# Performance work log

Hardware: AMD Instinct MI355X
Metric: run time of the kernel (lower is better)

## Reference

```python
import jax, jax.numpy as jnp
import numpy as np
from jax import lax

T, R, W, F_CWT, E, H, HG, NC, K = 16, 200, 50, 32, 128, 256, 256, 2, 20


def _make_wavelets():
    t = np.linspace(-1.0, 1.0, W)
    w0 = 6.0
    freqs = np.linspace(1.0, W / 2.0, F_CWT)
    wr = np.zeros((F_CWT, 1, W), np.float32)
    wi = np.zeros((F_CWT, 1, W), np.float32)
    for i, s in enumerate(freqs):
        norm = s ** (-0.5) * np.pi ** (-0.25)
        ts = t / s
        psi = norm * np.exp(1j * w0 * ts) * np.exp(-0.5 * ts ** 2)
        wr[i, 0] = psi.real.astype(np.float32)
        wi[i, 0] = psi.imag.astype(np.float32)
    return jnp.asarray(wr), jnp.asarray(wi)


def setup_inputs() -> dict:
    key = jax.random.key(0)
    ks = jax.random.split(key, 20)
    wr, wi = _make_wavelets()
    s = 0.05
    inp = {
        "time_windows": jax.random.normal(ks[0], (T, R, W), jnp.float32),
        "wav_real": wr, "wav_imag": wi,
        "conv1_w": jax.random.normal(ks[1], (16, 1, 3, 3), jnp.float32) * s,
        "conv1_b": jnp.zeros((16,), jnp.float32),
        "bn1_g": jnp.ones((16,), jnp.float32), "bn1_b": jnp.zeros((16,), jnp.float32),
        "conv2_w": jax.random.normal(ks[2], (32, 16, 3, 3), jnp.float32) * s,
        "conv2_b": jnp.zeros((32,), jnp.float32),
        "bn2_g": jnp.ones((32,), jnp.float32), "bn2_b": jnp.zeros((32,), jnp.float32),
        "fc_w": jax.random.normal(ks[3], (E, 32), jnp.float32) * s,
        "fc_b": jnp.zeros((E,), jnp.float32),
        "q_w": jax.random.normal(ks[4], (E, E), jnp.float32) * s,
        "q_b": jnp.zeros((E,), jnp.float32),
        "k_w": jax.random.normal(ks[5], (E, E), jnp.float32) * s,
        "k_b": jnp.zeros((E,), jnp.float32),
        "gcn1_w": jax.random.normal(ks[6], (E, H), jnp.float32) * s,
        "gcn1_b": jnp.zeros((H,), jnp.float32),
        "gcn2_w": jax.random.normal(ks[7], (H, H), jnp.float32) * s,
        "gcn2_b": jnp.zeros((H,), jnp.float32),
        "gru_wih": jax.random.normal(ks[8], (3 * HG, H), jnp.float32) * s,
        "gru_whh": jax.random.normal(ks[9], (3 * HG, HG), jnp.float32) * s,
        "gru_bih": jnp.zeros((3 * HG,), jnp.float32),
        "gru_bhh": jnp.zeros((3 * HG,), jnp.float32),
        "cls_w": jax.random.normal(ks[10], (NC, HG), jnp.float32) * s,
        "cls_b": jnp.zeros((NC,), jnp.float32),
    }
    return inp


def _conv_bn_relu_pool(x, w, b, g, beta):
    # conv2d k3 pad1, training-mode BN, relu, maxpool2 (floor)
    x = lax.conv_general_dilated(x, w, (1, 1), ((1, 1), (1, 1)),
                                 dimension_numbers=("NCHW", "OIHW", "NCHW"))
    x = x + b[None, :, None, None]
    mu = x.mean((0, 2, 3), keepdims=True)
    var = x.var((0, 2, 3), keepdims=True)
    x = (x - mu) * lax.rsqrt(var + 1e-5) * g[None, :, None, None] + beta[None, :, None, None]
    x = jax.nn.relu(x)
    return lax.reduce_window(x, -jnp.inf, lax.max, (1, 1, 2, 2), (1, 1, 2, 2), "VALID")


def _forward(time_windows, wav_real, wav_imag, conv1_w, conv1_b, bn1_g, bn1_b,
             conv2_w, conv2_b, bn2_g, bn2_b, fc_w, fc_b, q_w, q_b, k_w, k_b,
             gcn1_w, gcn1_b, gcn2_w, gcn2_b, gru_wih, gru_whh, gru_bih, gru_bhh,
             cls_w, cls_b):
    N = T * R
    x = time_windows.reshape(N, 1, W)
    pl = (W - 1) // 2
    pr = (W - 1) - pl  # torch padding='same' (extra on right)
    re = lax.conv_general_dilated(x, wav_real, (1,), [(pl, pr)],
                                  dimension_numbers=("NCH", "OIH", "NCH"))
    im = lax.conv_general_dilated(x, wav_imag, (1,), [(pl, pr)],
                                  dimension_numbers=("NCH", "OIH", "NCH"))
    scal = jnp.sqrt(re * re + im * im)              # [N, F_CWT, W]

    h = scal[:, None]                               # [N,1,F,W]
    h = _conv_bn_relu_pool(h, conv1_w, conv1_b, bn1_g, bn1_b)
    h = _conv_bn_relu_pool(h, conv2_w, conv2_b, bn2_g, bn2_b)
    pooled = h.mean((2, 3))                         # adaptive avg pool -> [N,32]
    emb = pooled @ fc_w.T + fc_b                    # [N,E]
    emb = emb.reshape(T, R, E)

    # sparse-attention graph generation (per window, vectorized over T)
    Q = emb @ q_w.T + q_b
    Kp = emb @ k_w.T + k_b
    attn = jnp.einsum("tre,tse->trs", Q, Kp) / (E ** 0.5)
    attn = jax.nn.leaky_relu(attn, 0.2)
    _, idx = lax.top_k(attn, K)                     # [T,R,K]
    mask = jnp.zeros_like(attn).at[
        jnp.arange(T)[:, None, None], jnp.arange(R)[None, :, None], idx].set(1.0)
    masked = attn * mask
    masked = jnp.where(masked == 0.0, -1e9, masked)
    adj = jax.nn.softmax(masked, axis=-1)           # [T,R,R] row-stochastic, topk-sparse

    # GCNConv x2 with edge weights (PyG gcn_norm: remaining self-loops weight 1,
    ii = jnp.arange(R)
    diag = adj[:, ii, ii]
    adj_sl = adj.at[:, ii, ii].set(jnp.where(diag == 0.0, 1.0, diag))
    Bm = jnp.swapaxes(adj_sl, 1, 2)
    deg = Bm.sum(-1)
    dinv = jnp.where(deg > 0, deg, 1.0) ** -0.5
    An = dinv[:, :, None] * Bm * dinv[:, None, :]   # [T,R,R]
    g = jax.nn.relu(jnp.einsum("trs,tsh->trh", An, emb @ gcn1_w) + gcn1_b)
    g = jax.nn.relu(jnp.einsum("trs,tsh->trh", An, g @ gcn2_w) + gcn2_b)
    g_emb = g.mean(1)                               # [T,H]

    # GRU over the T graph embeddings (batch 1, gate order r,z,n)
    def step(hprev, xt):
        gi = xt @ gru_wih.T + gru_bih
        gh = hprev @ gru_whh.T + gru_bhh
        ir, iz, inn = jnp.split(gi, 3)
        hr, hz, hn = jnp.split(gh, 3)
        r = jax.nn.sigmoid(ir + hr)
        z = jax.nn.sigmoid(iz + hz)
        n = jnp.tanh(inn + r * hn)
        return (1.0 - z) * n + z * hprev, None

    hT, _ = lax.scan(step, jnp.zeros((HG,), emb.dtype), g_emb)
    pred = (hT @ cls_w.T + cls_b)[None]             # [1,NC]

    edge_var = jnp.mean(jnp.var(adj, axis=0, ddof=1))
    avg_adj = adj.mean(0)[None]                     # [1,R,R]
    return pred, avg_adj, edge_var


def reference(time_windows, wav_real, wav_imag, conv1_w, conv1_b, bn1_g, bn1_b,
              conv2_w, conv2_b, bn2_g, bn2_b, fc_w, fc_b, q_w, q_b, k_w, k_b,
              gcn1_w, gcn1_b, gcn2_w, gcn2_b, gru_wih, gru_whh, gru_bih, gru_bhh,
              cls_w, cls_b):
    return _forward(time_windows, wav_real, wav_imag, conv1_w, conv1_b, bn1_g, bn1_b,
                    conv2_w, conv2_b, bn2_g, bn2_b, fc_w, fc_b, q_w, q_b, k_w, k_b,
                    gcn1_w, gcn1_b, gcn2_w, gcn2_b, gru_wih, gru_whh, gru_bih, gru_bhh,
                    cls_w, cls_b)
```

## Files before the change

kernel.cpp:

```cpp
#include <hip/hip_runtime.h>
#include <cfloat>
#include <cmath>

#define T_ 16
#define R_ 200
#define W_ 50
#define FCWT 32
#define E_ 128
#define K_ 20
#define N_ 3200

__device__ __forceinline__ void waveReduce2(float& a, float& b) {
#pragma unroll
    for (int o = 32; o > 0; o >>= 1) {
        a += __shfl_down(a, o, 64);
        b += __shfl_down(b, o, 64);
    }
}

__global__ __launch_bounds__(256) void cwt_conv1_stats_kernel(const float* __restrict__ x,
                                                              const float* __restrict__ wr,
                                                              const float* __restrict__ wi,
                                                              const float* __restrict__ w1,
                                                              const float* __restrict__ b1,
                                                              float* __restrict__ scal,
                                                              double* __restrict__ psum,
                                                              double* __restrict__ psq) {
    int n = blockIdx.x, tid = threadIdx.x;
    __shared__ float sx[W_];
    __shared__ float swr[FCWT * W_];
    __shared__ float swi[FCWT * W_];
    __shared__ float P1[34 * 52];
    __shared__ float ls[256], lq[256];
    if (tid < W_) sx[tid] = x[n * W_ + tid];
    for (int idx = tid; idx < FCWT * W_; idx += 256) { swr[idx] = wr[idx]; swi[idx] = wi[idx]; }
    for (int idx = tid; idx < 34 * 52; idx += 256) P1[idx] = 0.f;
    __syncthreads();
    for (int idx = tid; idx < 1600; idx += 256) {
        int f = idx / 50, i = idx % 50;
        int jlo = (24 - i) > 0 ? (24 - i) : 0;
        int jhi = (73 - i) < 49 ? (73 - i) : 49;
        float re = 0.f, im = 0.f;
        for (int j = jlo; j <= jhi; ++j) {
            float xv = sx[i + j - 24];
            re += xv * swr[f * 50 + j];
            im += xv * swi[f * 50 + j];
        }
        float v = sqrtf(re * re + im * im);
        scal[n * 1600 + idx] = v;
        P1[(f + 1) * 52 + (i + 1)] = v;
    }
    __syncthreads();
    int c = tid & 15, pgq = tid >> 4;
    float wv[9];
#pragma unroll
    for (int j = 0; j < 9; ++j) wv[j] = w1[c * 9 + j];
    float bias = b1[c];
    float s = 0.f, q = 0.f;
    for (int k = 0; k < 100; ++k) {
        int pos = pgq + 16 * k;
        int y = pos / 50, xx = pos % 50;
        const float* p = &P1[y * 52 + xx];
        float v = bias + p[0] * wv[0] + p[1] * wv[1] + p[2] * wv[2]
                       + p[52] * wv[3] + p[53] * wv[4] + p[54] * wv[5]
                       + p[104] * wv[6] + p[105] * wv[7] + p[106] * wv[8];
        s += v; q += v * v;
    }
    ls[tid] = s; lq[tid] = q;
    __syncthreads();
    if (tid < 16) {
        float ss = 0.f, qq = 0.f;
        for (int g = 0; g < 16; ++g) { ss += ls[tid + 16 * g]; qq += lq[tid + 16 * g]; }
        psum[n * 16 + tid] = (double)ss;
        psq[n * 16 + tid] = (double)qq;
    }
}

__global__ __launch_bounds__(256) void bn_finalize_kernel(const double* __restrict__ psum,
                                                          const double* __restrict__ psq,
                                                          const float* __restrict__ g,
                                                          const float* __restrict__ beta,
                                                          float* __restrict__ scale,
                                                          float* __restrict__ shift,
                                                          int C, double inv_count) {
    int c = blockIdx.x, tid = threadIdx.x;
    double s = 0.0, q = 0.0;
    for (int n = tid; n < N_; n += 256) { s += psum[n * C + c]; q += psq[n * C + c]; }
#pragma unroll
    for (int o = 32; o > 0; o >>= 1) { s += __shfl_down(s, o, 64); q += __shfl_down(q, o, 64); }
    __shared__ double sa[4], sb[4];
    int lane = tid & 63, wid = tid >> 6;
    if (lane == 0) { sa[wid] = s; sb[wid] = q; }
    __syncthreads();
    if (tid == 0) {
        s = sa[0] + sa[1] + sa[2] + sa[3];
        q = sb[0] + sb[1] + sb[2] + sb[3];
        double mu = s * inv_count;
        double var = q * inv_count - mu * mu;
        double rstd = 1.0 / sqrt(var + 1e-5);
        double gg = (double)g[c];
        scale[c] = (float)(gg * rstd);
        shift[c] = (float)((double)beta[c] - mu * rstd * gg);
    }
}

__global__ __launch_bounds__(256) void conv1_norm_pool_kernel(const float* __restrict__ scal,
                                                              const float* __restrict__ w1,
                                                              const float* __restrict__ b1,
                                                              const float* __restrict__ scale,
                                                              const float* __restrict__ shift,
                                                              float* __restrict__ pooled1) {
    int n = blockIdx.x, tid = threadIdx.x;
    __shared__ float P1[34 * 52];
    for (int idx = tid; idx < 34 * 52; idx += 256) {
        int yy = idx / 52, xx = idx % 52;
        float v = 0.f;
        if (yy >= 1 && yy <= 32 && xx >= 1 && xx <= 50)
            v = scal[n * 1600 + (yy - 1) * 50 + (xx - 1)];
        P1[idx] = v;
    }
    __syncthreads();
    int c = tid >> 4, sub = tid & 15;
    float wv[9];
#pragma unroll
    for (int j = 0; j < 9; ++j) wv[j] = w1[c * 9 + j];
    float bias = b1[c], sc = scale[c], sh = shift[c];
    for (int k = 0; k < 25; ++k) {
        int cell = sub + 16 * k;
        int py = cell / 25, px = cell % 25;
        int y0 = 2 * py, x0 = 2 * px;
        float p[4][4];
#pragma unroll
        for (int iy = 0; iy < 4; ++iy)
#pragma unroll
            for (int ix = 0; ix < 4; ++ix)
                p[iy][ix] = P1[(y0 + iy) * 52 + x0 + ix];
        float m = -FLT_MAX;
#pragma unroll
        for (int dy = 0; dy < 2; ++dy)
#pragma unroll
            for (int dx = 0; dx < 2; ++dx) {
                float acc = bias;
#pragma unroll
                for (int ky = 0; ky < 3; ++ky)
#pragma unroll
                    for (int kx = 0; kx < 3; ++kx)
                        acc += p[dy + ky][dx + kx] * wv[ky * 3 + kx];
                m = fmaxf(m, acc * sc + sh);
            }
        pooled1[((n * 16 + c) * 16 + py) * 25 + px] = fmaxf(m, 0.f);
    }
}

__global__ __launch_bounds__(256) void conv2_compute_kernel(const float* __restrict__ pooled1,
                                                            const float* __restrict__ w2,
                                                            const float* __restrict__ b2,
                                                            float* __restrict__ mm,
                                                            double* __restrict__ psum,
                                                            double* __restrict__ psq,
                                                            int store_min) {
    int n = blockIdx.x, tid = threadIdx.x;
    __shared__ float P2[16 * 18 * 27];
    __shared__ float swT[144 * 32];
    __shared__ float ls[256], lq[256];
    for (int idx = tid; idx < 16 * 18 * 27; idx += 256) {
        int ci = idx / 486, rem = idx % 486, yy = rem / 27, xx = rem % 27;
        float v = 0.f;
        if (yy >= 1 && yy <= 16 && xx >= 1 && xx <= 25)
            v = pooled1[((n * 16 + ci) * 16 + (yy - 1)) * 25 + (xx - 1)];
        P2[idx] = v;
    }
    for (int idx = tid; idx < 4608; idx += 256) {
        int co = idx / 144, r = idx % 144;
        swT[r * 32 + co] = w2[idx];
    }
    __syncthreads();
    int co = tid & 31, pg = tid >> 5;
    float bias = b2[co];
    float s = 0.f, q = 0.f;
    int stride = store_min ? 64 : 32;
    for (int kk = 0; kk < 4; ++kk) {
        int task = pg + 8 * kk;
        int pr = task >> 2, cb = task & 3;
        int y0 = 2 * pr, x0 = 6 * cb;
        float a[2][6];
#pragma unroll
        for (int r2 = 0; r2 < 2; ++r2)
#pragma unroll
            for (int xi = 0; xi < 6; ++xi) a[r2][xi] = bias;
        for (int ci = 0; ci < 16; ++ci) {
            const float* base = &P2[ci * 486];
            const float* wb = &swT[(ci * 9) * 32 + co];
#pragma unroll
            for (int iy = 0; iy < 4; ++iy) {
                const float* row = &base[(y0 + iy) * 27 + x0];
                float r0 = row[0], r1 = row[1], r2v = row[2], r3 = row[3];
                float r4 = row[4], r5 = row[5], r6 = row[6], r7 = row[7];
                if (iy < 3) {
                    float w0 = wb[(iy * 3 + 0) * 32], w1 = wb[(iy * 3 + 1) * 32], w2v = wb[(iy * 3 + 2) * 32];
                    a[0][0] += r0 * w0 + r1 * w1 + r2v * w2v;
                    a[0][1] += r1 * w0 + r2v * w1 + r3 * w2v;
                    a[0][2] += r2v * w0 + r3 * w1 + r4 * w2v;
                    a[0][3] += r3 * w0 + r4 * w1 + r5 * w2v;
                    a[0][4] += r4 * w0 + r5 * w1 + r6 * w2v;
                    a[0][5] += r5 * w0 + r6 * w1 + r7 * w2v;
                }
                if (iy >= 1) {
                    int ky = iy - 1;
                    float w0 = wb[(ky * 3 + 0) * 32], w1 = wb[(ky * 3 + 1) * 32], w2v = wb[(ky * 3 + 2) * 32];
                    a[1][0] += r0 * w0 + r1 * w1 + r2v * w2v;
                    a[1][1] += r1 * w0 + r2v * w1 + r3 * w2v;
                    a[1][2] += r2v * w0 + r3 * w1 + r4 * w2v;
                    a[1][3] += r3 * w0 + r4 * w1 + r5 * w2v;
                    a[1][4] += r4 * w0 + r5 * w1 + r6 * w2v;
                    a[1][5] += r5 * w0 + r6 * w1 + r7 * w2v;
                }
            }
        }
#pragma unroll
        for (int r2 = 0; r2 < 2; ++r2)
#pragma unroll
            for (int xi = 0; xi < 6; ++xi) { float v = a[r2][xi]; s += v; q += v * v; }
#pragma unroll
        for (int pc = 0; pc < 3; ++pc) {
            float v00 = a[0][2 * pc], v01 = a[0][2 * pc + 1];
            float v10 = a[1][2 * pc], v11 = a[1][2 * pc + 1];
            float mx = fmaxf(fmaxf(v00, v01), fmaxf(v10, v11));
            int cellIdx = pr * 12 + 3 * cb + pc;
            mm[((size_t)n * 96 + cellIdx) * stride + co] = mx;
            if (store_min) {
                float mn = fminf(fminf(v00, v01), fminf(v10, v11));
                mm[((size_t)n * 96 + cellIdx) * 64 + 32 + co] = mn;
            }
        }
    }
    {
        int y0 = 2 * pg;
        float a0 = bias, a1 = bias;
        for (int ci = 0; ci < 16; ++ci) {
            const float* base = &P2[ci * 486];
            const float* wb = &swT[(ci * 9) * 32 + co];
#pragma unroll
            for (int iy = 0; iy < 4; ++iy) {
                const float* row = &base[(y0 + iy) * 27 + 24];
                float r0 = row[0], r1 = row[1], r2v = row[2];
                if (iy < 3) {
                    float w0 = wb[(iy * 3 + 0) * 32], w1 = wb[(iy * 3 + 1) * 32], w2v = wb[(iy * 3 + 2) * 32];
                    a0 += r0 * w0 + r1 * w1 + r2v * w2v;
                }
                if (iy >= 1) {
                    int ky = iy - 1;
                    float w0 = wb[(ky * 3 + 0) * 32], w1 = wb[(ky * 3 + 1) * 32], w2v = wb[(ky * 3 + 2) * 32];
                    a1 += r0 * w0 + r1 * w1 + r2v * w2v;
                }
            }
        }
        s += a0 + a1; q += a0 * a0 + a1 * a1;
    }
    ls[tid] = s; lq[tid] = q;
    __syncthreads();
    if (tid < 32) {
        float ss = 0.f, qq = 0.f;
        for (int g2 = 0; g2 < 8; ++g2) { ss += ls[tid + 32 * g2]; qq += lq[tid + 32 * g2]; }
        psum[n * 32 + tid] = (double)ss;
        psq[n * 32 + tid] = (double)qq;
    }
}

__global__ __launch_bounds__(256) void pool_mean_kernel(const float* __restrict__ mm,
                                                        const float* __restrict__ scale,
                                                        const float* __restrict__ shift,
                                                        float* __restrict__ pm,
                                                        int store_min) {
    int n = blockIdx.x, tid = threadIdx.x;
    int co = tid & 31, grp = tid >> 5;
    float sc = scale[co], sh = shift[co];
    int stride = store_min ? 64 : 32;
    float acc = 0.f;
    for (int j = 0; j < 12; ++j) {
        int cell = grp * 12 + j;
        float v;
        if (store_min && sc < 0.f) {
            float mn = mm[((size_t)n * 96 + cell) * 64 + 32 + co];
            v = mn * sc + sh;
        } else {
            float mx = mm[((size_t)n * 96 + cell) * stride + co];
            v = mx * sc + sh;
        }
        acc += fmaxf(v, 0.f);
    }
    __shared__ float red[256];
    red[tid] = acc;
    __syncthreads();
    if (tid < 32) {
        float t = 0.f;
        for (int g = 0; g < 8; ++g) t += red[co + 32 * g];
        pm[n * 32 + co] = t * (1.f / 96.f);
    }
}

__global__ __launch_bounds__(128) void fc_kernel(const float* __restrict__ pm,
                                                 const float* __restrict__ fc_w,
                                                 const float* __restrict__ fc_b,
                                                 float* __restrict__ emb) {
    int n = blockIdx.x, e = threadIdx.x;
    __shared__ float sp[32];
    if (e < 32) sp[e] = pm[n * 32 + e];
    __syncthreads();
    const float* w = fc_w + e * 32;
    float acc = fc_b[e];
    for (int c = 0; c < 32; ++c) acc += sp[c] * w[c];
    emb[n * 128 + e] = acc;
}

__global__ __launch_bounds__(128) void qk_kernel(const float* __restrict__ emb,
                                                 const float* __restrict__ q_w,
                                                 const float* __restrict__ q_b,
                                                 const float* __restrict__ k_w,
                                                 const float* __restrict__ k_b,
                                                 float* __restrict__ Q,
                                                 float* __restrict__ Kp) {
    int n = blockIdx.x, e = threadIdx.x;
    const float* w = (blockIdx.y == 0) ? q_w : k_w;
    const float* b = (blockIdx.y == 0) ? q_b : k_b;
    float* out = (blockIdx.y == 0) ? Q : Kp;
    __shared__ float se[128];
    se[e] = emb[n * 128 + e];
    __syncthreads();
    const float* wr = w + e * 128;
    float acc = b[e];
    for (int k = 0; k < 128; ++k) acc += se[k] * wr[k];
    out[n * 128 + e] = acc;
}

__global__ __launch_bounds__(256) void attn_kernel(const float* __restrict__ Q,
                                                   const float* __restrict__ Kp,
                                                   float* __restrict__ attn) {
    int r = blockIdx.x, t = blockIdx.y, tid = threadIdx.x;
    __shared__ float sq[128];
    if (tid < 128) sq[tid] = Q[(t * 200 + r) * 128 + tid];
    __syncthreads();
    if (tid < 200) {
        const float4* kp4 = (const float4*)(Kp + (size_t)(t * 200 + tid) * 128);
        float acc = 0.f;
#pragma unroll 8
        for (int e4 = 0; e4 < 32; ++e4) {
            float4 k4 = kp4[e4];
            acc += sq[e4 * 4 + 0] * k4.x + sq[e4 * 4 + 1] * k4.y +
                   sq[e4 * 4 + 2] * k4.z + sq[e4 * 4 + 3] * k4.w;
        }
        acc = acc / 11.313708498984761f;
        acc = (acc >= 0.f) ? acc : 0.2f * acc;
        attn[(size_t)(t * 200 + r) * 200 + tid] = acc;
    }
}

__global__ __launch_bounds__(64) void topk_softmax_kernel(const float* __restrict__ attn,
                                                          float* __restrict__ adj) {
    int row = blockIdx.x;
    int lane = threadIdx.x;
    const float* a = attn + (size_t)row * 200;
    float v[4], w[4];
#pragma unroll
    for (int j = 0; j < 4; ++j) {
        int i = lane + 64 * j;
        float x = (i < 200) ? a[i] : -FLT_MAX;
        v[j] = x; w[j] = x;
    }
    unsigned sel = 0;
    for (int it = 0; it < K_; ++it) {
        float best = -FLT_MAX; int bidx = 0x7fffffff;
#pragma unroll
        for (int j = 0; j < 4; ++j) {
            int i = lane + 64 * j;
            if (w[j] > best || (w[j] == best && i < bidx)) { best = w[j]; bidx = i; }
        }
#pragma unroll
        for (int off = 32; off > 0; off >>= 1) {
            float ob = __shfl_down(best, off, 64);
            int oi = __shfl_down(bidx, off, 64);
            if (ob > best || (ob == best && oi < bidx)) { best = ob; bidx = oi; }
        }
        bidx = __shfl(bidx, 0, 64);
        if ((bidx & 63) == lane) { int j = bidx >> 6; w[j] = -FLT_MAX; sel |= (1u << j); }
    }
    float mv[4]; float m = -FLT_MAX;
#pragma unroll
    for (int j = 0; j < 4; ++j) {
        int i = lane + 64 * j;
        float x = -1e9f;
        if (i < 200 && ((sel >> j) & 1u)) x = (v[j] == 0.f) ? -1e9f : v[j];
        mv[j] = x; m = fmaxf(m, x);
    }
#pragma unroll
    for (int off = 32; off > 0; off >>= 1) m = fmaxf(m, __shfl_xor(m, off, 64));
    float s = 0.f; float e[4];
#pragma unroll
    for (int j = 0; j < 4; ++j) {
        int i = lane + 64 * j;
        e[j] = (i < 200) ? expf(mv[j] - m) : 0.f;
        s += e[j];
    }
#pragma unroll
    for (int off = 32; off > 0; off >>= 1) s += __shfl_xor(s, off, 64);
    float inv = 1.f / s;
#pragma unroll
    for (int j = 0; j < 4; ++j) {
        int i = lane + 64 * j;
        if (i < 200) adj[(size_t)row * 200 + i] = e[j] * inv;
    }
}

__global__ __launch_bounds__(256) void build_An_kernel(const float* __restrict__ adj,
                                                       float* __restrict__ An) {
    int t = blockIdx.x, tid = threadIdx.x;
    __shared__ float dinv[200];
    if (tid < 200) {
        float acc = 0.f;
        for (int s = 0; s < 200; ++s) {
            float v = adj[(size_t)(t * 200 + s) * 200 + tid];
            if (s == tid) v = (v == 0.f) ? 1.f : v;
            acc += v;
        }
        float d = (acc > 0.f) ? acc : 1.f;
        dinv[tid] = 1.f / sqrtf(d);
    }
    __syncthreads();
    for (int idx = tid; idx < 200 * 200; idx += 256) {
        int r = idx / 200, s = idx % 200;
        float v = adj[(size_t)(t * 200 + s) * 200 + r];
        if (s == r) v = (v == 0.f) ? 1.f : v;
        An[(size_t)(t * 200 + r) * 200 + s] = dinv[r] * v * dinv[s];
    }
}

__global__ __launch_bounds__(256) void linear_kernel(const float* __restrict__ in,
                                                     const float* __restrict__ w,
                                                     float* __restrict__ out, int IN) {
    int n = blockIdx.x, h = threadIdx.x;
    __shared__ float s[256];
    for (int i = h; i < IN; i += 256) s[i] = in[n * IN + i];
    __syncthreads();
    float acc = 0.f;
    for (int k = 0; k < IN; ++k) acc += s[k] * w[k * 256 + h];
    out[(size_t)n * 256 + h] = acc;
}

__global__ __launch_bounds__(256) void gcn_agg_kernel(const float* __restrict__ An,
                                                      const float* __restrict__ X,
                                                      const float* __restrict__ b,
                                                      float* __restrict__ out) {
    int r = blockIdx.x, t = blockIdx.y, h = threadIdx.x;
    __shared__ float sa[200];
    for (int i = h; i < 200; i += 256) sa[i] = An[(size_t)(t * 200 + r) * 200 + i];
    __syncthreads();
    const float* Xt = X + (size_t)t * 200 * 256;
    float acc = 0.f;
    for (int s = 0; s < 200; ++s) acc += sa[s] * Xt[s * 256 + h];
    out[(size_t)(t * 200 + r) * 256 + h] = fmaxf(acc + b[h], 0.f);
}

__global__ __launch_bounds__(256) void gemb_kernel(const float* __restrict__ g2,
                                                   float* __restrict__ g_emb) {
    int t = blockIdx.x, h = threadIdx.x;
    float acc = 0.f;
    for (int r = 0; r < 200; ++r) acc += g2[(size_t)(t * 200 + r) * 256 + h];
    g_emb[t * 256 + h] = acc * (1.f / 200.f);
}

__global__ __launch_bounds__(256) void transpose_768x256_kernel(const float* __restrict__ in,
                                                                float* __restrict__ outT) {
    int gid = blockIdx.x * 256 + threadIdx.x;
    int k = gid / 768, j = gid % 768;
    outT[gid] = in[j * 256 + k];
}

__global__ __launch_bounds__(768) void gi_kernel(const float* __restrict__ g_emb,
                                                 const float* __restrict__ wihT,
                                                 const float* __restrict__ bih,
                                                 float* __restrict__ GI) {
    int t = blockIdx.x, j = threadIdx.x;
    __shared__ float sg[256];
    if (j < 256) sg[j] = g_emb[t * 256 + j];
    __syncthreads();
    float acc = bih[j];
    for (int k = 0; k < 256; ++k) acc += sg[k] * wihT[k * 768 + j];
    GI[t * 768 + j] = acc;
}

__global__ __launch_bounds__(768) void gru_cls_kernel(const float* __restrict__ GI,
                                                      const float* __restrict__ whhT,
                                                      const float* __restrict__ bhh,
                                                      const float* __restrict__ cls_w,
                                                      const float* __restrict__ cls_b,
                                                      float* __restrict__ out) {
    int j = threadIdx.x;
    __shared__ float h[256];
    __shared__ float gh[768];
    __shared__ float s0[4], s1[4];
    if (j < 256) h[j] = 0.f;
    float bh = bhh[j];
    __syncthreads();
    for (int t = 0; t < 16; ++t) {
        float acc = bh;
        for (int k = 0; k < 256; ++k) acc += h[k] * whhT[k * 768 + j];
        gh[j] = acc;
        __syncthreads();
        if (j < 256) {
            float r = 1.f / (1.f + expf(-(GI[t * 768 + j] + gh[j])));
            float z = 1.f / (1.f + expf(-(GI[t * 768 + 256 + j] + gh[256 + j])));
            float nn = tanhf(GI[t * 768 + 512 + j] + r * gh[512 + j]);
            h[j] = (1.f - z) * nn + z * h[j];
        }
        __syncthreads();
    }
    float v0 = 0.f, v1 = 0.f;
    if (j < 256) { v0 = h[j] * cls_w[j]; v1 = h[j] * cls_w[256 + j]; }
    waveReduce2(v0, v1);
    int lane = j & 63, wid = j >> 6;
    if (lane == 0 && wid < 4) { s0[wid] = v0; s1[wid] = v1; }
    __syncthreads();
    if (j == 0) {
        out[0] = s0[0] + s0[1] + s0[2] + s0[3] + cls_b[0];
        out[1] = s1[0] + s1[1] + s1[2] + s1[3] + cls_b[1];
    }
}

__global__ __launch_bounds__(256) void edge_kernel(const float* __restrict__ adj,
                                                   float* __restrict__ out) {
    int gid = blockIdx.x * 256 + threadIdx.x;
    float var = 0.f;
    if (gid < 40000) {
        float v[16]; float s = 0.f;
#pragma unroll
        for (int t = 0; t < 16; ++t) { v[t] = adj[t * 40000 + gid]; s += v[t]; }
        float mean = s * (1.f / 16.f);
        float q = 0.f;
#pragma unroll
        for (int t = 0; t < 16; ++t) { float d = v[t] - mean; q += d * d; }
        var = q * (1.f / 15.f);
        out[2 + gid] = mean;
    }
    float dummy = 0.f;
    waveReduce2(var, dummy);
    __shared__ float sa[4];
    int lane = threadIdx.x & 63, wid = threadIdx.x >> 6;
    if (lane == 0) sa[wid] = var;
    __syncthreads();
    if (threadIdx.x == 0) {
        float bs = sa[0] + sa[1] + sa[2] + sa[3];
        atomicAdd(&out[40002], bs * (1.f / 40000.f));
    }
}

extern "C" void kernel_launch(void* const* d_in, const int* in_sizes, int n_in,
                              void* d_out, int out_size, void* d_ws, size_t ws_size,
                              hipStream_t stream) {
    const float* tw      = (const float*)d_in[0];
    const float* wav_r   = (const float*)d_in[1];
    const float* wav_i   = (const float*)d_in[2];
    const float* conv1_w = (const float*)d_in[3];
    const float* conv1_b = (const float*)d_in[4];
    const float* bn1_g   = (const float*)d_in[5];
    const float* bn1_b   = (const float*)d_in[6];
    const float* conv2_w = (const float*)d_in[7];
    const float* conv2_b = (const float*)d_in[8];
    const float* bn2_g   = (const float*)d_in[9];
    const float* bn2_b   = (const float*)d_in[10];
    const float* fc_w    = (const float*)d_in[11];
    const float* fc_b    = (const float*)d_in[12];
    const float* q_w     = (const float*)d_in[13];
    const float* q_b     = (const float*)d_in[14];
    const float* k_w     = (const float*)d_in[15];
    const float* k_b     = (const float*)d_in[16];
    const float* gcn1_w  = (const float*)d_in[17];
    const float* gcn1_b  = (const float*)d_in[18];
    const float* gcn2_w  = (const float*)d_in[19];
    const float* gcn2_b  = (const float*)d_in[20];
    const float* gru_wih = (const float*)d_in[21];
    const float* gru_whh = (const float*)d_in[22];
    const float* gru_bih = (const float*)d_in[23];
    const float* gru_bhh = (const float*)d_in[24];
    const float* cls_w   = (const float*)d_in[25];
    const float* cls_b   = (const float*)d_in[26];
    float* out = (float*)d_out;
    (void)in_sizes; (void)n_in; (void)out_size;

    const size_t POOLED1_B = (size_t)N_ * 16 * 16 * 25 * 4;
    const size_t SCALU_B   = (size_t)N_ * 1600 * 4;
    const size_t MM_FULL_B = (size_t)N_ * 96 * 64 * 4;
    const size_t MM_MAX_B  = (size_t)N_ * 96 * 32 * 4;
    const size_t P1S_B     = (size_t)N_ * 16 * 8;
    const size_t P2S_B     = (size_t)N_ * 32 * 8;
    const size_t WT_B      = (size_t)768 * 256 * 4;
    size_t fixed = POOLED1_B + SCALU_B + 2 * P1S_B + 2 * P2S_B + 2 * WT_B + 8 * 256 + 4096;
    int store_min = (ws_size >= fixed + MM_FULL_B) ? 1 : 0;
    const size_t MM_B = store_min ? MM_FULL_B : MM_MAX_B;

    size_t off = 0;
    char* Wb = (char*)d_ws;
    auto take = [&](size_t bytes) -> char* {
        char* p = Wb + off;
        off += (bytes + 255) & ~(size_t)255;
        return p;
    };
    float* pooled1 = (float*)take(POOLED1_B);
    char*  scalU   = take(SCALU_B);
    char*  mmU     = take(MM_B);
    double* p1sum = (double*)take(P1S_B);
    double* p1sq  = (double*)take(P1S_B);
    double* p2sum = (double*)take(P2S_B);
    double* p2sq  = (double*)take(P2S_B);
    float* scale1 = (float*)take(64 * 4);
    float* shift1 = (float*)take(64 * 4);
    float* scale2 = (float*)take(64 * 4);
    float* shift2 = (float*)take(64 * 4);
    float* wihT   = (float*)take(WT_B);
    float* whhT   = (float*)take(WT_B);

    float* scal = (float*)scalU;
    float* pm   = (float*)(scalU + 0);
    float* emb  = (float*)(scalU + 409600);
    float* Q    = (float*)(scalU + 409600 + 1638400);
    float* Kp   = (float*)(scalU + 409600 + 2 * 1638400);

    float* mm   = (float*)mmU;
    size_t moff = 0;
    auto mtake = [&](size_t bytes) -> float* {
        float* p = (float*)(mmU + moff);
        moff += (bytes + 255) & ~(size_t)255;
        return p;
    };
    float* attn  = mtake((size_t)T_ * 200 * 200 * 4);
    float* adj   = mtake((size_t)T_ * 200 * 200 * 4);
    float* An    = mtake((size_t)T_ * 200 * 200 * 4);
    float* X1    = mtake((size_t)N_ * 256 * 4);
    float* g1    = mtake((size_t)N_ * 256 * 4);
    float* X2    = mtake((size_t)N_ * 256 * 4);
    float* g2    = mtake((size_t)N_ * 256 * 4);
    float* g_emb = mtake((size_t)T_ * 256 * 4);
    float* GI    = mtake((size_t)T_ * 768 * 4);

    transpose_768x256_kernel<<<768, 256, 0, stream>>>(gru_wih, wihT);
    transpose_768x256_kernel<<<768, 256, 0, stream>>>(gru_whh, whhT);
    cwt_conv1_stats_kernel<<<N_, 256, 0, stream>>>(tw, wav_r, wav_i, conv1_w, conv1_b,
                                                   scal, p1sum, p1sq);
    bn_finalize_kernel<<<16, 256, 0, stream>>>(p1sum, p1sq, bn1_g, bn1_b, scale1, shift1,
                                               16, 1.0 / 5120000.0);
    conv1_norm_pool_kernel<<<N_, 256, 0, stream>>>(scal, conv1_w, conv1_b, scale1, shift1,
                                                   pooled1);
    conv2_compute_kernel<<<N_, 256, 0, stream>>>(pooled1, conv2_w, conv2_b, mm,
                                                 p2sum, p2sq, store_min);
    bn_finalize_kernel<<<32, 256, 0, stream>>>(p2sum, p2sq, bn2_g, bn2_b, scale2, shift2,
                                               32, 1.0 / 1280000.0);
    pool_mean_kernel<<<N_, 256, 0, stream>>>(mm, scale2, shift2, pm, store_min);
    fc_kernel<<<N_, 128, 0, stream>>>(pm, fc_w, fc_b, emb);
    qk_kernel<<<dim3(N_, 2), 128, 0, stream>>>(emb, q_w, q_b, k_w, k_b, Q, Kp);
    attn_kernel<<<dim3(200, 16), 256, 0, stream>>>(Q, Kp, attn);
    topk_softmax_kernel<<<N_, 64, 0, stream>>>(attn, adj);
    build_An_kernel<<<16, 256, 0, stream>>>(adj, An);
    linear_kernel<<<N_, 256, 0, stream>>>(emb, gcn1_w, X1, 128);
    gcn_agg_kernel<<<dim3(200, 16), 256, 0, stream>>>(An, X1, gcn1_b, g1);
    linear_kernel<<<N_, 256, 0, stream>>>(g1, gcn2_w, X2, 256);
    gcn_agg_kernel<<<dim3(200, 16), 256, 0, stream>>>(An, X2, gcn2_b, g2);
    gemb_kernel<<<16, 256, 0, stream>>>(g2, g_emb);
    gi_kernel<<<16, 768, 0, stream>>>(g_emb, wihT, gru_bih, GI);
    gru_cls_kernel<<<1, 768, 0, stream>>>(GI, whhT, gru_bhh, cls_w, cls_b, out);
    hipMemsetAsync(out + 40002, 0, sizeof(float), stream);
    edge_kernel<<<(40000 + 255) / 256, 256, 0, stream>>>(adj, out);
}
```

Before: 903.0 us.

## Restructure conv, GCN and GRU kernels for register reuse and multi-block recurrence

Rewrites the CWT as a sliding-window register computation and changes conv1 stats and conv1-pool to row-streaming sliding windows with pooled output staged in shared memory. conv2 now computes whole output rows per thread with float4 loads. Building the normalized adjacency is split into a degree kernel and a tiled transpose kernel. The linear and GCN aggregation kernels process 8 rows per block so each loaded weight or feature is reused. The GRU recurrence is spread over 6 blocks with register-resident weights and a flag-based inter-block barrier, which adds spin-wait synchronisation risk and extra register pressure.

```diff
diff --git a/kernel.cpp b/kernel.cpp
--- a/kernel.cpp
+++ b/kernel.cpp
@@ -9,6 +9,7 @@
 #define E_ 128
 #define K_ 20
 #define N_ 3200
+#define GRU_BLOCKS 6
 
 __device__ __forceinline__ void waveReduce2(float& a, float& b) {
 #pragma unroll
@@ -27,44 +28,67 @@
                                                               double* __restrict__ psum,
                                                               double* __restrict__ psq) {
     int n = blockIdx.x, tid = threadIdx.x;
-    __shared__ float sx[W_];
+    __shared__ float sxp[112];
     __shared__ float swr[FCWT * W_];
     __shared__ float swi[FCWT * W_];
     __shared__ float P1[34 * 52];
     __shared__ float ls[256], lq[256];
-    if (tid < W_) sx[tid] = x[n * W_ + tid];
+    if (tid < 112) sxp[tid] = (tid >= 24 && tid < 74) ? x[n * 50 + (tid - 24)] : 0.f;
     for (int idx = tid; idx < FCWT * W_; idx += 256) { swr[idx] = wr[idx]; swi[idx] = wi[idx]; }
     for (int idx = tid; idx < 34 * 52; idx += 256) P1[idx] = 0.f;
     __syncthreads();
+    if (tid < 64) {
+        int f = tid >> 1, i0 = (tid & 1) * 25;
+        float xw[25], ar[25], ai[25];
+#pragma unroll
+        for (int d = 0; d < 25; ++d) { xw[d] = sxp[i0 + d]; ar[d] = 0.f; ai[d] = 0.f; }
+        const float* wrf = &swr[f * 50];
+        const float* wif = &swi[f * 50];
+        for (int j = 0; j < 50; ++j) {
+            float wrv = wrf[j], wiv = wif[j];
+#pragma unroll
+            for (int d = 0; d < 25; ++d) { ar[d] += xw[d] * wrv; ai[d] += xw[d] * wiv; }
+            float xnew = sxp[i0 + j + 25];
+#pragma unroll
+            for (int d = 0; d < 24; ++d) xw[d] = xw[d + 1];
+            xw[24] = xnew;
+        }
+#pragma unroll
+        for (int d = 0; d < 25; ++d) {
+            float v = sqrtf(ar[d] * ar[d] + ai[d] * ai[d]);
+            P1[(f + 1) * 52 + (i0 + d + 1)] = v;
+        }
+    }
+    __syncthreads();
     for (int idx = tid; idx < 1600; idx += 256) {
-        int f = idx / 50, i = idx % 50;
-        int jlo = (24 - i) > 0 ? (24 - i) : 0;
-        int jhi = (73 - i) < 49 ? (73 - i) : 49;
-        float re = 0.f, im = 0.f;
-        for (int j = jlo; j <= jhi; ++j) {
-            float xv = sx[i + j - 24];
-            re += xv * swr[f * 50 + j];
-            im += xv * swi[f * 50 + j];
-        }
-        float v = sqrtf(re * re + im * im);
-        scal[n * 1600 + idx] = v;
-        P1[(f + 1) * 52 + (i + 1)] = v;
-    }
-    __syncthreads();
-    int c = tid & 15, pgq = tid >> 4;
+        int ff = idx / 50, ii = idx % 50;
+        scal[n * 1600 + idx] = P1[(ff + 1) * 52 + ii + 1];
+    }
+    int c = tid & 15, pg = tid >> 4;
     float wv[9];
 #pragma unroll
-    for (int j = 0; j < 9; ++j) wv[j] = w1[c * 9 + j];
+    for (int k = 0; k < 9; ++k) wv[k] = w1[c * 9 + k];
     float bias = b1[c];
+    const float* r0p = &P1[(2 * pg + 0) * 52];
+    const float* r1p = &P1[(2 * pg + 1) * 52];
+    const float* r2p = &P1[(2 * pg + 2) * 52];
+    const float* r3p = &P1[(2 * pg + 3) * 52];
+    float c0[4], c1[4];
+    c0[0] = r0p[0]; c0[1] = r1p[0]; c0[2] = r2p[0]; c0[3] = r3p[0];
+    c1[0] = r0p[1]; c1[1] = r1p[1]; c1[2] = r2p[1]; c1[3] = r3p[1];
     float s = 0.f, q = 0.f;
-    for (int k = 0; k < 100; ++k) {
-        int pos = pgq + 16 * k;
-        int y = pos / 50, xx = pos % 50;
-        const float* p = &P1[y * 52 + xx];
-        float v = bias + p[0] * wv[0] + p[1] * wv[1] + p[2] * wv[2]
-                       + p[52] * wv[3] + p[53] * wv[4] + p[54] * wv[5]
-                       + p[104] * wv[6] + p[105] * wv[7] + p[106] * wv[8];
-        s += v; q += v * v;
+    for (int xx = 0; xx < 50; ++xx) {
+        float c2[4];
+        c2[0] = r0p[xx + 2]; c2[1] = r1p[xx + 2]; c2[2] = r2p[xx + 2]; c2[3] = r3p[xx + 2];
+        float v0 = bias + c0[0] * wv[0] + c1[0] * wv[1] + c2[0] * wv[2]
+                        + c0[1] * wv[3] + c1[1] * wv[4] + c2[1] * wv[5]
+                        + c0[2] * wv[6] + c1[2] * wv[7] + c2[2] * wv[8];
+        float v1 = bias + c0[1] * wv[0] + c1[1] * wv[1] + c2[1] * wv[2]
+                        + c0[2] * wv[3] + c1[2] * wv[4] + c2[2] * wv[5]
+                        + c0[3] * wv[6] + c1[3] * wv[7] + c2[3] * wv[8];
+        s += v0 + v1; q += v0 * v0 + v1 * v1;
+#pragma unroll
+        for (int rr = 0; rr < 4; ++rr) { c0[rr] = c1[rr]; c1[rr] = c2[rr]; }
     }
     ls[tid] = s; lq[tid] = q;
     __syncthreads();
@@ -112,6 +136,7 @@
                                                               float* __restrict__ pooled1) {
     int n = blockIdx.x, tid = threadIdx.x;
     __shared__ float P1[34 * 52];
+    __shared__ float outb[6400];
     for (int idx = tid; idx < 34 * 52; idx += 256) {
         int yy = idx / 52, xx = idx % 52;
         float v = 0.f;
@@ -120,36 +145,37 @@
         P1[idx] = v;
     }
     __syncthreads();
-    int c = tid >> 4, sub = tid & 15;
+    int c = tid & 15, py = tid >> 4;
     float wv[9];
 #pragma unroll
-    for (int j = 0; j < 9; ++j) wv[j] = w1[c * 9 + j];
+    for (int k = 0; k < 9; ++k) wv[k] = w1[c * 9 + k];
     float bias = b1[c], sc = scale[c], sh = shift[c];
-    for (int k = 0; k < 25; ++k) {
-        int cell = sub + 16 * k;
-        int py = cell / 25, px = cell % 25;
-        int y0 = 2 * py, x0 = 2 * px;
-        float p[4][4];
-#pragma unroll
-        for (int iy = 0; iy < 4; ++iy)
-#pragma unroll
-            for (int ix = 0; ix < 4; ++ix)
-                p[iy][ix] = P1[(y0 + iy) * 52 + x0 + ix];
-        float m = -FLT_MAX;
-#pragma unroll
-        for (int dy = 0; dy < 2; ++dy)
-#pragma unroll
-            for (int dx = 0; dx < 2; ++dx) {
-                float acc = bias;
-#pragma unroll
-                for (int ky = 0; ky < 3; ++ky)
-#pragma unroll
-                    for (int kx = 0; kx < 3; ++kx)
-                        acc += p[dy + ky][dx + kx] * wv[ky * 3 + kx];
-                m = fmaxf(m, acc * sc + sh);
-            }
-        pooled1[((n * 16 + c) * 16 + py) * 25 + px] = fmaxf(m, 0.f);
-    }
+    const float* r0p = &P1[(2 * py + 0) * 52];
+    const float* r1p = &P1[(2 * py + 1) * 52];
+    const float* r2p = &P1[(2 * py + 2) * 52];
+    const float* r3p = &P1[(2 * py + 3) * 52];
+    float c0[4], c1[4];
+    c0[0] = r0p[0]; c0[1] = r1p[0]; c0[2] = r2p[0]; c0[3] = r3p[0];
+    c1[0] = r0p[1]; c1[1] = r1p[1]; c1[2] = r2p[1]; c1[3] = r3p[1];
+    float pmax = -FLT_MAX;
+    for (int xx = 0; xx < 50; ++xx) {
+        float c2[4];
+        c2[0] = r0p[xx + 2]; c2[1] = r1p[xx + 2]; c2[2] = r2p[xx + 2]; c2[3] = r3p[xx + 2];
+        float v0 = bias + c0[0] * wv[0] + c1[0] * wv[1] + c2[0] * wv[2]
+                        + c0[1] * wv[3] + c1[1] * wv[4] + c2[1] * wv[5]
+                        + c0[2] * wv[6] + c1[2] * wv[7] + c2[2] * wv[8];
+        float v1 = bias + c0[1] * wv[0] + c1[1] * wv[1] + c2[1] * wv[2]
+                        + c0[2] * wv[3] + c1[2] * wv[4] + c2[2] * wv[5]
+                        + c0[3] * wv[6] + c1[3] * wv[7] + c2[3] * wv[8];
+        float m2 = fmaxf(v0 * sc + sh, v1 * sc + sh);
+        if ((xx & 1) == 0) pmax = m2;
+        else outb[(c * 16 + py) * 25 + (xx >> 1)] = fmaxf(fmaxf(pmax, m2), 0.f);
+#pragma unroll
+        for (int rr = 0; rr < 4; ++rr) { c0[rr] = c1[rr]; c1[rr] = c2[rr]; }
+    }
+    __syncthreads();
+    for (int idx = tid; idx < 6400; idx += 256)
+        pooled1[(size_t)n * 6400 + idx] = outb[idx];
 }
 
 __global__ __launch_bounds__(256) void conv2_compute_kernel(const float* __restrict__ pooled1,
@@ -160,14 +186,14 @@
                                                             double* __restrict__ psq,
                                                             int store_min) {
     int n = blockIdx.x, tid = threadIdx.x;
-    __shared__ float P2[16 * 18 * 27];
+    __shared__ float P2[16 * 18 * 28];
     __shared__ float swT[144 * 32];
     __shared__ float ls[256], lq[256];
-    for (int idx = tid; idx < 16 * 18 * 27; idx += 256) {
-        int ci = idx / 486, rem = idx % 486, yy = rem / 27, xx = rem % 27;
+    for (int idx = tid; idx < 16 * 18 * 28; idx += 256) {
+        int ci = idx / 504, rem = idx % 504, yy = rem / 28, xx = rem % 28;
         float v = 0.f;
         if (yy >= 1 && yy <= 16 && xx >= 1 && xx <= 25)
-            v = pooled1[((n * 16 + ci) * 16 + (yy - 1)) * 25 + (xx - 1)];
+            v = pooled1[((size_t)n * 16 + ci) * 400 + (yy - 1) * 25 + (xx - 1)];
         P2[idx] = v;
     }
     for (int idx = tid; idx < 4608; idx += 256) {
@@ -177,85 +203,56 @@
     __syncthreads();
     int co = tid & 31, pg = tid >> 5;
     float bias = b2[co];
+    float acc0[25], acc1[25];
+#pragma unroll
+    for (int cv = 0; cv < 25; ++cv) { acc0[cv] = bias; acc1[cv] = bias; }
+    for (int ci = 0; ci < 16; ++ci) {
+        const float* wb = &swT[ci * 288 + co];
+        float w[9];
+#pragma unroll
+        for (int k = 0; k < 9; ++k) w[k] = wb[k * 32];
+        const float* base = &P2[ci * 504 + (2 * pg) * 28];
+#pragma unroll
+        for (int iy = 0; iy < 4; ++iy) {
+            float r[28];
+            const float4* rp = (const float4*)(base + iy * 28);
+#pragma unroll
+            for (int m = 0; m < 7; ++m) {
+                float4 v4 = rp[m];
+                r[4 * m] = v4.x; r[4 * m + 1] = v4.y; r[4 * m + 2] = v4.z; r[4 * m + 3] = v4.w;
+            }
+            if (iy < 3) {
+                int kb = iy * 3;
+#pragma unroll
+                for (int cv = 0; cv < 25; ++cv)
+                    acc0[cv] += r[cv] * w[kb] + r[cv + 1] * w[kb + 1] + r[cv + 2] * w[kb + 2];
+            }
+            if (iy >= 1) {
+                int kb = (iy - 1) * 3;
+#pragma unroll
+                for (int cv = 0; cv < 25; ++cv)
+                    acc1[cv] += r[cv] * w[kb] + r[cv + 1] * w[kb + 1] + r[cv + 2] * w[kb + 2];
+            }
+        }
+    }
     float s = 0.f, q = 0.f;
+#pragma unroll
+    for (int cv = 0; cv < 25; ++cv) {
+        s += acc0[cv] + acc1[cv];
+        q += acc0[cv] * acc0[cv] + acc1[cv] * acc1[cv];
+    }
     int stride = store_min ? 64 : 32;
-    for (int kk = 0; kk < 4; ++kk) {
-        int task = pg + 8 * kk;
-        int pr = task >> 2, cb = task & 3;
-        int y0 = 2 * pr, x0 = 6 * cb;
-        float a[2][6];
-#pragma unroll
-        for (int r2 = 0; r2 < 2; ++r2)
-#pragma unroll
-            for (int xi = 0; xi < 6; ++xi) a[r2][xi] = bias;
-        for (int ci = 0; ci < 16; ++ci) {
-            const float* base = &P2[ci * 486];
-            const float* wb = &swT[(ci * 9) * 32 + co];
-#pragma unroll
-            for (int iy = 0; iy < 4; ++iy) {
-                const float* row = &base[(y0 + iy) * 27 + x0];
-                float r0 = row[0], r1 = row[1], r2v = row[2], r3 = row[3];
-                float r4 = row[4], r5 = row[5], r6 = row[6], r7 = row[7];
-                if (iy < 3) {
-                    float w0 = wb[(iy * 3 + 0) * 32], w1 = wb[(iy * 3 + 1) * 32], w2v = wb[(iy * 3 + 2) * 32];
-                    a[0][0] += r0 * w0 + r1 * w1 + r2v * w2v;
-                    a[0][1] += r1 * w0 + r2v * w1 + r3 * w2v;
-                    a[0][2] += r2v * w0 + r3 * w1 + r4 * w2v;
-                    a[0][3] += r3 * w0 + r4 * w1 + r5 * w2v;
-                    a[0][4] += r4 * w0 + r5 * w1 + r6 * w2v;
-                    a[0][5] += r5 * w0 + r6 * w1 + r7 * w2v;
-                }
-                if (iy >= 1) {
-                    int ky = iy - 1;
-                    float w0 = wb[(ky * 3 + 0) * 32], w1 = wb[(ky * 3 + 1) * 32], w2v = wb[(ky * 3 + 2) * 32];
-                    a[1][0] += r0 * w0 + r1 * w1 + r2v * w2v;
-                    a[1][1] += r1 * w0 + r2v * w1 + r3 * w2v;
-                    a[1][2] += r2v * w0 + r3 * w1 + r4 * w2v;
-                    a[1][3] += r3 * w0 + r4 * w1 + r5 * w2v;
-                    a[1][4] += r4 * w0 + r5 * w1 + r6 * w2v;
-                    a[1][5] += r5 * w0 + r6 * w1 + r7 * w2v;
-                }
-            }
-        }
-#pragma unroll
-        for (int r2 = 0; r2 < 2; ++r2)
-#pragma unroll
-            for (int xi = 0; xi < 6; ++xi) { float v = a[r2][xi]; s += v; q += v * v; }
-#pragma unroll
-        for (int pc = 0; pc < 3; ++pc) {
-            float v00 = a[0][2 * pc], v01 = a[0][2 * pc + 1];
-            float v10 = a[1][2 * pc], v11 = a[1][2 * pc + 1];
-            float mx = fmaxf(fmaxf(v00, v01), fmaxf(v10, v11));
-            int cellIdx = pr * 12 + 3 * cb + pc;
-            mm[((size_t)n * 96 + cellIdx) * stride + co] = mx;
-            if (store_min) {
-                float mn = fminf(fminf(v00, v01), fminf(v10, v11));
-                mm[((size_t)n * 96 + cellIdx) * 64 + 32 + co] = mn;
-            }
-        }
-    }
-    {
-        int y0 = 2 * pg;
-        float a0 = bias, a1 = bias;
-        for (int ci = 0; ci < 16; ++ci) {
-            const float* base = &P2[ci * 486];
-            const float* wb = &swT[(ci * 9) * 32 + co];
-#pragma unroll
-            for (int iy = 0; iy < 4; ++iy) {
-                const float* row = &base[(y0 + iy) * 27 + 24];
-                float r0 = row[0], r1 = row[1], r2v = row[2];
-                if (iy < 3) {
-                    float w0 = wb[(iy * 3 + 0) * 32], w1 = wb[(iy * 3 + 1) * 32], w2v = wb[(iy * 3 + 2) * 32];
-                    a0 += r0 * w0 + r1 * w1 + r2v * w2v;
-                }
-                if (iy >= 1) {
-                    int ky = iy - 1;
-                    float w0 = wb[(ky * 3 + 0) * 32], w1 = wb[(ky * 3 + 1) * 32], w2v = wb[(ky * 3 + 2) * 32];
-                    a1 += r0 * w0 + r1 * w1 + r2v * w2v;
-                }
-            }
-        }
-        s += a0 + a1; q += a0 * a0 + a1 * a1;
+#pragma unroll
+    for (int pc = 0; pc < 12; ++pc) {
+        float v00 = acc0[2 * pc], v01 = acc0[2 * pc + 1];
+        float v10 = acc1[2 * pc], v11 = acc1[2 * pc + 1];
+        float mx = fmaxf(fmaxf(v00, v01), fmaxf(v10, v11));
+        int cell = pg * 12 + pc;
+        mm[((size_t)n * 96 + cell) * stride + co] = mx;
+        if (store_min) {
+            float mn = fminf(fminf(v00, v01), fminf(v10, v11));
+            mm[((size_t)n * 96 + cell) * 64 + 32 + co] = mn;
+        }
     }
     ls[tid] = s; lq[tid] = q;
     __syncthreads();
@@ -411,10 +408,9 @@
     }
 }
 
-__global__ __launch_bounds__(256) void build_An_kernel(const float* __restrict__ adj,
-                                                       float* __restrict__ An) {
+__global__ __launch_bounds__(256) void deg_kernel(const float* __restrict__ adj,
+                                                  float* __restrict__ dinv) {
     int t = blockIdx.x, tid = threadIdx.x;
-    __shared__ float dinv[200];
     if (tid < 200) {
         float acc = 0.f;
         for (int s = 0; s < 200; ++s) {
@@ -423,41 +419,75 @@
             acc += v;
         }
         float d = (acc > 0.f) ? acc : 1.f;
-        dinv[tid] = 1.f / sqrtf(d);
-    }
-    __syncthreads();
-    for (int idx = tid; idx < 200 * 200; idx += 256) {
-        int r = idx / 200, s = idx % 200;
-        float v = adj[(size_t)(t * 200 + s) * 200 + r];
-        if (s == r) v = (v == 0.f) ? 1.f : v;
-        An[(size_t)(t * 200 + r) * 200 + s] = dinv[r] * v * dinv[s];
-    }
-}
-
-__global__ __launch_bounds__(256) void linear_kernel(const float* __restrict__ in,
-                                                     const float* __restrict__ w,
-                                                     float* __restrict__ out, int IN) {
-    int n = blockIdx.x, h = threadIdx.x;
-    __shared__ float s[256];
-    for (int i = h; i < IN; i += 256) s[i] = in[n * IN + i];
-    __syncthreads();
-    float acc = 0.f;
-    for (int k = 0; k < IN; ++k) acc += s[k] * w[k * 256 + h];
-    out[(size_t)n * 256 + h] = acc;
+        dinv[t * 200 + tid] = 1.f / sqrtf(d);
+    }
+}
+
+__global__ __launch_bounds__(256) void an_tile_kernel(const float* __restrict__ adj,
+                                                      const float* __restrict__ dinv,
+                                                      float* __restrict__ An) {
+    int t = blockIdx.y;
+    int tr = blockIdx.x >> 2, tc = blockIdx.x & 3;
+    int r0 = tr * 50, s0 = tc * 50;
+    int tid = threadIdx.x;
+    __shared__ float Tt[50 * 51];
+    __shared__ float dr[50], ds[50];
+    for (int idx = tid; idx < 2500; idx += 256) {
+        int a = idx / 50, b = idx % 50;
+        Tt[a * 51 + b] = adj[(size_t)(t * 200 + s0 + a) * 200 + r0 + b];
+    }
+    if (tid < 50) dr[tid] = dinv[t * 200 + r0 + tid];
+    else if (tid >= 64 && tid < 114) ds[tid - 64] = dinv[t * 200 + s0 + (tid - 64)];
+    __syncthreads();
+    for (int idx = tid; idx < 2500; idx += 256) {
+        int rl = idx / 50, sl = idx % 50;
+        float v = Tt[sl * 51 + rl];
+        if (r0 + rl == s0 + sl) v = (v == 0.f) ? 1.f : v;
+        An[(size_t)(t * 200 + r0 + rl) * 200 + s0 + sl] = dr[rl] * v * ds[sl];
+    }
+}
+
+__global__ __launch_bounds__(256) void linear8_kernel(const float* __restrict__ in,
+                                                      const float* __restrict__ w,
+                                                      float* __restrict__ out, int IN) {
+    int n0 = blockIdx.x * 8, h = threadIdx.x;
+    __shared__ float sin_[8 * 256];
+    for (int idx = h; idx < 8 * IN; idx += 256) sin_[idx] = in[(size_t)n0 * IN + idx];
+    __syncthreads();
+    float acc[8];
+#pragma unroll
+    for (int m = 0; m < 8; ++m) acc[m] = 0.f;
+    for (int k = 0; k < IN; ++k) {
+        float wv = w[k * 256 + h];
+#pragma unroll
+        for (int m = 0; m < 8; ++m) acc[m] += sin_[m * IN + k] * wv;
+    }
+#pragma unroll
+    for (int m = 0; m < 8; ++m) out[(size_t)(n0 + m) * 256 + h] = acc[m];
 }
 
 __global__ __launch_bounds__(256) void gcn_agg_kernel(const float* __restrict__ An,
                                                       const float* __restrict__ X,
                                                       const float* __restrict__ b,
                                                       float* __restrict__ out) {
-    int r = blockIdx.x, t = blockIdx.y, h = threadIdx.x;
-    __shared__ float sa[200];
-    for (int i = h; i < 200; i += 256) sa[i] = An[(size_t)(t * 200 + r) * 200 + i];
+    int t = blockIdx.y, r0 = blockIdx.x * 8, h = threadIdx.x;
+    __shared__ float sa[8 * 200];
+    for (int idx = h; idx < 1600; idx += 256)
+        sa[idx] = An[(size_t)(t * 200 + r0) * 200 + idx];
     __syncthreads();
     const float* Xt = X + (size_t)t * 200 * 256;
-    float acc = 0.f;
-    for (int s = 0; s < 200; ++s) acc += sa[s] * Xt[s * 256 + h];
-    out[(size_t)(t * 200 + r) * 256 + h] = fmaxf(acc + b[h], 0.f);
+    float acc[8];
+#pragma unroll
+    for (int m = 0; m < 8; ++m) acc[m] = 0.f;
+    for (int s = 0; s < 200; ++s) {
+        float xv = Xt[s * 256 + h];
+#pragma unroll
+        for (int m = 0; m < 8; ++m) acc[m] += sa[m * 200 + s] * xv;
+    }
+    float bb = b[h];
+#pragma unroll
+    for (int m = 0; m < 8; ++m)
+        out[(size_t)(t * 200 + r0 + m) * 256 + h] = fmaxf(acc[m] + bb, 0.f);
 }
 
 __global__ __launch_bounds__(256) void gemb_kernel(const float* __restrict__ g2,
@@ -488,41 +518,70 @@
     GI[t * 768 + j] = acc;
 }
 
-__global__ __launch_bounds__(768) void gru_cls_kernel(const float* __restrict__ GI,
+__global__ __launch_bounds__(256) void gru_cls_kernel(const float* __restrict__ GI,
                                                       const float* __restrict__ whhT,
                                                       const float* __restrict__ bhh,
                                                       const float* __restrict__ cls_w,
                                                       const float* __restrict__ cls_b,
+                                                      float* __restrict__ GH,
+                                                      int* __restrict__ flags,
                                                       float* __restrict__ out) {
-    int j = threadIdx.x;
-    __shared__ float h[256];
-    __shared__ float gh[768];
+    int b = blockIdx.x, tid = threadIdx.x;
+    int jl = tid & 127;
+    int kc = tid >> 7;
+    int j = b * 128 + jl;
+    float wreg[128];
+#pragma unroll 16
+    for (int k = 0; k < 128; ++k)
+        wreg[k] = whhT[(size_t)(kc * 128 + k) * 768 + j];
+    __shared__ float hcur[256];
+    __shared__ float part[256];
     __shared__ float s0[4], s1[4];
-    if (j < 256) h[j] = 0.f;
-    float bh = bhh[j];
-    __syncthreads();
-    for (int t = 0; t < 16; ++t) {
-        float acc = bh;
-        for (int k = 0; k < 256; ++k) acc += h[k] * whhT[k * 768 + j];
-        gh[j] = acc;
+    hcur[tid] = 0.f;
+    __syncthreads();
+    for (int st = 0; st < 16; ++st) {
+        float p = 0.f;
+        const float* hb = &hcur[kc * 128];
+#pragma unroll 16
+        for (int k = 0; k < 128; ++k) p += hb[k] * wreg[k];
+        part[tid] = p;
         __syncthreads();
-        if (j < 256) {
-            float r = 1.f / (1.f + expf(-(GI[t * 768 + j] + gh[j])));
-            float z = 1.f / (1.f + expf(-(GI[t * 768 + 256 + j] + gh[256 + j])));
-            float nn = tanhf(GI[t * 768 + 512 + j] + r * gh[512 + j]);
-            h[j] = (1.f - z) * nn + z * h[j];
-        }
+        if (tid < 128) {
+            GH[st * 768 + b * 128 + tid] = part[tid] + part[tid + 128];
+        }
+        __threadfence();
         __syncthreads();
-    }
-    float v0 = 0.f, v1 = 0.f;
-    if (j < 256) { v0 = h[j] * cls_w[j]; v1 = h[j] * cls_w[256 + j]; }
-    waveReduce2(v0, v1);
-    int lane = j & 63, wid = j >> 6;
-    if (lane == 0 && wid < 4) { s0[wid] = v0; s1[wid] = v1; }
-    __syncthreads();
-    if (j == 0) {
-        out[0] = s0[0] + s0[1] + s0[2] + s0[3] + cls_b[0];
-        out[1] = s1[0] + s1[1] + s1[2] + s1[3] + cls_b[1];
+        if (tid == 0)
+            __hip_atomic_store(&flags[b], st + 1, __ATOMIC_RELEASE, __HIP_MEMORY_SCOPE_AGENT);
+        for (int bb = 0; bb < GRU_BLOCKS; ++bb) {
+            while (__hip_atomic_load(&flags[bb], __ATOMIC_ACQUIRE, __HIP_MEMORY_SCOPE_AGENT) <= st)
+                __builtin_amdgcn_s_sleep(2);
+        }
+        float ghr = GH[st * 768 + tid]       + bhh[tid];
+        float ghz = GH[st * 768 + 256 + tid] + bhh[256 + tid];
+        float ghn = GH[st * 768 + 512 + tid] + bhh[512 + tid];
+        float gir = GI[st * 768 + tid];
+        float giz = GI[st * 768 + 256 + tid];
+        float gin = GI[st * 768 + 512 + tid];
+        float r = 1.f / (1.f + expf(-(gir + ghr)));
+        float z = 1.f / (1.f + expf(-(giz + ghz)));
+        float nn = tanhf(gin + r * ghn);
+        float hnew = (1.f - z) * nn + z * hcur[tid];
+        __syncthreads();
+        hcur[tid] = hnew;
+        __syncthreads();
+    }
+    if (b == 0) {
+        float v0 = hcur[tid] * cls_w[tid];
+        float v1 = hcur[tid] * cls_w[256 + tid];
+        waveReduce2(v0, v1);
+        int lane = tid & 63, wid = tid >> 6;
+        if (lane == 0) { s0[wid] = v0; s1[wid] = v1; }
+        __syncthreads();
+        if (tid == 0) {
+            out[0] = s0[0] + s0[1] + s0[2] + s0[3] + cls_b[0];
+            out[1] = s1[0] + s1[1] + s1[2] + s1[3] + cls_b[1];
+        }
     }
 }
 
@@ -593,7 +652,7 @@
     const size_t P1S_B     = (size_t)N_ * 16 * 8;
     const size_t P2S_B     = (size_t)N_ * 32 * 8;
     const size_t WT_B      = (size_t)768 * 256 * 4;
-    size_t fixed = POOLED1_B + SCALU_B + 2 * P1S_B + 2 * P2S_B + 2 * WT_B + 8 * 256 + 4096;
+    size_t fixed = POOLED1_B + SCALU_B + 2 * P1S_B + 2 * P2S_B + 2 * WT_B + 8 * 256 + 65536;
     int store_min = (ws_size >= fixed + MM_FULL_B) ? 1 : 0;
     const size_t MM_B = store_min ? MM_FULL_B : MM_MAX_B;
 
@@ -617,6 +676,9 @@
     float* shift2 = (float*)take(64 * 4);
     float* wihT   = (float*)take(WT_B);
     float* whhT   = (float*)take(WT_B);
+    float* dinv   = (float*)take((size_t)T_ * 200 * 4);
+    float* GH     = (float*)take((size_t)16 * 768 * 4);
+    int*   flags  = (int*)take(256);
 
     float* scal = (float*)scalU;
     float* pm   = (float*)(scalU + 0);
@@ -658,14 +720,17 @@
     qk_kernel<<<dim3(N_, 2), 128, 0, stream>>>(emb, q_w, q_b, k_w, k_b, Q, Kp);
     attn_kernel<<<dim3(200, 16), 256, 0, stream>>>(Q, Kp, attn);
     topk_softmax_kernel<<<N_, 64, 0, stream>>>(attn, adj);
-    build_An_kernel<<<16, 256, 0, stream>>>(adj, An);
-    linear_kernel<<<N_, 256, 0, stream>>>(emb, gcn1_w, X1, 128);
-    gcn_agg_kernel<<<dim3(200, 16), 256, 0, stream>>>(An, X1, gcn1_b, g1);
-    linear_kernel<<<N_, 256, 0, stream>>>(g1, gcn2_w, X2, 256);
-    gcn_agg_kernel<<<dim3(200, 16), 256, 0, stream>>>(An, X2, gcn2_b, g2);
+    deg_kernel<<<16, 256, 0, stream>>>(adj, dinv);
+    an_tile_kernel<<<dim3(16, 16), 256, 0, stream>>>(adj, dinv, An);
+    linear8_kernel<<<N_ / 8, 256, 0, stream>>>(emb, gcn1_w, X1, 128);
+    gcn_agg_kernel<<<dim3(25, 16), 256, 0, stream>>>(An, X1, gcn1_b, g1);
+    linear8_kernel<<<N_ / 8, 256, 0, stream>>>(g1, gcn2_w, X2, 256);
+    gcn_agg_kernel<<<dim3(25, 16), 256, 0, stream>>>(An, X2, gcn2_b, g2);
     gemb_kernel<<<16, 256, 0, stream>>>(g2, g_emb);
     gi_kernel<<<16, 768, 0, stream>>>(g_emb, wihT, gru_bih, GI);
-    gru_cls_kernel<<<1, 768, 0, stream>>>(GI, whhT, gru_bhh, cls_w, cls_b, out);
+    hipMemsetAsync(flags, 0, 256, stream);
+    gru_cls_kernel<<<GRU_BLOCKS, 256, 0, stream>>>(GI, whhT, gru_bhh, cls_w, cls_b,
+                                                   GH, flags, out);
     hipMemsetAsync(out + 40002, 0, sizeof(float), stream);
     edge_kernel<<<(40000 + 255) / 256, 256, 0, stream>>>(adj, out);
 }
```

After: 865.8 us. 4.1% less time.
